# Optimization experiments

Hardware: AMD Instinct MI355X
Metric: run time of the kernel (lower is better)

Reference implementation:

```python
import jax, jax.numpy as jnp
import numpy as np

UNITS = 256
LB = -17.0
UB = 8.0
STEP = 0.05
NUM_BUCKETS = int((UB - LB) / STEP) + 1  # 501
RESIDUE = LB - STEP
W_INIT = 0.5
BATCH = 65536


def setup_inputs() -> dict:
    key = jax.random.key(0)
    kx, = jax.random.split(key, 1)
    x = jax.random.normal(kx, (BATCH, UNITS), dtype=jnp.float32)
    v = jnp.ones((UNITS, NUM_BUCKETS), dtype=jnp.float32) * W_INIT
    b = jnp.zeros((UNITS,), dtype=jnp.float32)
    return {"x": x, "v": v, "b": b}


def reference(x, v, b):
    # x: (batch, units); v: (units, num_buckets); b: (units,)
    x_clipped = jnp.clip(x, LB + 1e-9, UB - 1e-9)
    indx = ((x_clipped - LB + STEP) / STEP).astype(jnp.int32)
    indx = jnp.clip(indx, 0, NUM_BUCKETS - 1)  # (batch, units)
    delta = x_clipped - LB + STEP - indx.astype(x.dtype) * STEP

    w = jax.nn.relu(v)  # (units, num_buckets)
    # exclusive cumsum over buckets: csum[u, j] = sum_{k<j} w[u, k]
    csum = jnp.cumsum(w, axis=1)
    csum = jnp.concatenate([jnp.zeros((w.shape[0], 1), w.dtype), csum[:, :-1]], axis=1)

    unit_idx = jnp.arange(UNITS)[None, :]  # (1, units) broadcasts with indx
    csum_g = csum[unit_idx, indx]  # (batch, units)
    w_g = w[unit_idx, indx]        # (batch, units)

    # Equivalent to sum over buckets of (triangular step mask + scattered delta) * relu(v)
    logits = STEP * csum_g + delta * w_g + RESIDUE + b[None, :]
    return jax.nn.sigmoid(logits)
```

## Files before the change

kernel.cpp:

```cpp
#include <hip/hip_runtime.h>

#define UNITS 256
#define NB 501
#define STEPF 0.05f
#define LBF -17.0f
#define UBF 8.0f
#define RESIDUEF -17.05f
#define LOG2E 1.4426950408889634f

#define WLO 208
#define WSZ 224
#define UPB 32
#define PADF2 225
#define THREADS 1024
#define ROWS_PB 1024
#define CHUNKS 8

typedef float floatx4 __attribute__((ext_vector_type(4)));

__global__ __launch_bounds__(256) void build_table_kernel(
    const float* __restrict__ v, const float* __restrict__ b,
    float2* __restrict__ gtab) {
  const int lane = threadIdx.x & 63;
  const int wave = threadIdx.x >> 6;
  const int u = blockIdx.x * 4 + wave;
  if (u >= UNITS) return;

  const float* vu = v + u * NB;
  float w[8], pref[8];
  float run = 0.0f;
#pragma unroll
  for (int k = 0; k < 8; ++k) {
    const int j = lane * 8 + k;
    const float wv = (j < NB) ? fmaxf(vu[j], 0.0f) : 0.0f;
    w[k] = wv;
    pref[k] = run;
    run += wv;
  }
  float s = run;
#pragma unroll
  for (int d = 1; d < 64; d <<= 1) {
    const float o = __shfl_up(s, d, 64);
    if (lane >= d) s += o;
  }
  const float base = s - run;
  const float off = RESIDUEF + b[u];
#pragma unroll
  for (int k = 0; k < 8; ++k) {
    const int j = lane * 8 + k;
    if (j < NB) {
      const float C = STEPF * (base + pref[k]) + off - (float)j * STEPF * w[k];
      gtab[u * NB + j] = make_float2(C * LOG2E, w[k] * LOG2E);
    }
  }
}

__global__ __launch_bounds__(THREADS, 8) void iso_main_kernel(
    const float* __restrict__ x, const float2* __restrict__ gtab,
    float* __restrict__ out) {
  __shared__ float2 tab[UPB * PADF2];

  const int bu = blockIdx.x & 7;
  const int bb = blockIdx.x >> 3;
  const int u0 = bu * UPB;
  const int tid = threadIdx.x;

  {
    const int ul = tid >> 5;
    const int jt = tid & 31;
    const float2* __restrict__ src = gtab + (u0 + ul) * NB + WLO;
#pragma unroll
    for (int r = 0; r < 7; ++r) {
      const int j = jt + r * 32;
      tab[ul * PADF2 + j] = src[j];
    }
  }

  const int rowoff = tid >> 3;
  const int col4 = tid & 7;
  const floatx4* __restrict__ x4 = reinterpret_cast<const floatx4*>(x);
  floatx4* __restrict__ o4 = reinterpret_cast<floatx4*>(out);
  const int g0 = (bb * ROWS_PB + rowoff) * (UNITS / 4) + bu * (UPB / 4) + col4;
  const int gstep = 128 * (UNITS / 4);
  const int qbase = (col4 * 4) * PADF2;

  floatx4 xv[CHUNKS];
#pragma unroll
  for (int c = 0; c < CHUNKS; ++c) xv[c] = x4[g0 + c * gstep];
#pragma unroll
  for (int c = 0; c < CHUNKS; ++c) asm volatile("" : "+v"(xv[c]));

  __syncthreads();

#pragma unroll
  for (int c = 0; c < CHUNKS; ++c) {
    const floatx4 cur = xv[c];
    const float xs[4] = {cur.x, cur.y, cur.z, cur.w};
    float os[4];
#pragma unroll
    for (int k = 0; k < 4; ++k) {
      const float xc = fminf(fmaxf(xs[k], LBF + 1e-9f), UBF - 1e-9f);
      const float t = xc - LBF + STEPF;
      int idx = (int)(t * 20.0f);
      const unsigned iw = (unsigned)(idx - WLO);
      float2 cw;
      if (iw < WSZ) {
        cw = tab[qbase + k * PADF2 + (int)iw];
      } else {
        idx = idx < 0 ? 0 : (idx > NB - 1 ? NB - 1 : idx);
        cw = gtab[(u0 + col4 * 4 + k) * NB + idx];
      }
      const float l2 = fmaf(t, cw.y, cw.x);
      const float e = __builtin_amdgcn_exp2f(-l2);
      os[k] = __builtin_amdgcn_rcpf(1.0f + e);
    }
    floatx4 ov;
    ov.x = os[0]; ov.y = os[1]; ov.z = os[2]; ov.w = os[3];
    __builtin_nontemporal_store(ov, &o4[g0 + c * gstep]);
  }
}

extern "C" void kernel_launch(void* const* d_in, const int* in_sizes, int n_in,
                              void* d_out, int out_size, void* d_ws,
                              size_t ws_size, hipStream_t stream) {
  const float* x = (const float*)d_in[0];
  const float* v = (const float*)d_in[1];
  const float* b = (const float*)d_in[2];
  float* out = (float*)d_out;
  float2* gtab = (float2*)d_ws;

  build_table_kernel<<<64, 256, 0, stream>>>(v, b, gtab);

  const int rows = out_size / UNITS;
  const int grid = (UNITS / UPB) * (rows / ROWS_PB);
  iso_main_kernel<<<grid, THREADS, 0, stream>>>(x, gtab, out);
}
```

Before: 132.4 us.

## Store only cumulative sums and linearly interpolate between adjacent entries

The lookup table now holds one float per bucket (the scaled prefix sum) instead of a float2 pair of intercept and slope, and logits are formed by interpolating between neighbouring entries using the fractional part of the index. This halves table size in global and shared memory and the cost of filling the shared tile. Block size and rows per block are also halved to 512. Each evaluation now does two scalar LDS reads instead of one 8-byte read, and the interpolation may round slightly differently from the original formula.

Measured after the change: 136.7 us. 1.03x slower.

```diff
diff --git a/kernel.cpp b/kernel.cpp
--- a/kernel.cpp
+++ b/kernel.cpp
@@ -2,6 +2,7 @@
 
 #define UNITS 256
 #define NB 501
+#define NBA 502
 #define STEPF 0.05f
 #define LBF -17.0f
 #define UBF 8.0f
@@ -11,29 +12,28 @@
 #define WLO 208
 #define WSZ 224
 #define UPB 32
-#define PADF2 225
-#define THREADS 1024
-#define ROWS_PB 1024
+#define PADF 225
+#define THREADS 512
+#define ROWS_PB 512
 #define CHUNKS 8
 
 typedef float floatx4 __attribute__((ext_vector_type(4)));
 
 __global__ __launch_bounds__(256) void build_table_kernel(
     const float* __restrict__ v, const float* __restrict__ b,
-    float2* __restrict__ gtab) {
+    float* __restrict__ gtab) {
   const int lane = threadIdx.x & 63;
   const int wave = threadIdx.x >> 6;
   const int u = blockIdx.x * 4 + wave;
   if (u >= UNITS) return;
 
   const float* vu = v + u * NB;
-  float w[8], pref[8];
+  float pref[8];
   float run = 0.0f;
 #pragma unroll
   for (int k = 0; k < 8; ++k) {
     const int j = lane * 8 + k;
     const float wv = (j < NB) ? fmaxf(vu[j], 0.0f) : 0.0f;
-    w[k] = wv;
     pref[k] = run;
     run += wv;
   }
@@ -48,17 +48,16 @@
 #pragma unroll
   for (int k = 0; k < 8; ++k) {
     const int j = lane * 8 + k;
-    if (j < NB) {
-      const float C = STEPF * (base + pref[k]) + off - (float)j * STEPF * w[k];
-      gtab[u * NB + j] = make_float2(C * LOG2E, w[k] * LOG2E);
+    if (j < NBA) {
+      gtab[u * NBA + j] = (STEPF * (base + pref[k]) + off) * LOG2E;
     }
   }
 }
 
 __global__ __launch_bounds__(THREADS, 8) void iso_main_kernel(
-    const float* __restrict__ x, const float2* __restrict__ gtab,
+    const float* __restrict__ x, const float* __restrict__ gtab,
     float* __restrict__ out) {
-  __shared__ float2 tab[UPB * PADF2];
+  __shared__ float tab[UPB * PADF];
 
   const int bu = blockIdx.x & 7;
   const int bb = blockIdx.x >> 3;
@@ -66,14 +65,16 @@
   const int tid = threadIdx.x;
 
   {
-    const int ul = tid >> 5;
-    const int jt = tid & 31;
-    const float2* __restrict__ src = gtab + (u0 + ul) * NB + WLO;
+    const int ul = tid >> 4;
+    const int jt = tid & 15;
+    const float* __restrict__ src = gtab + (u0 + ul) * NBA + WLO;
+    float* __restrict__ dst = tab + ul * PADF;
 #pragma unroll
-    for (int r = 0; r < 7; ++r) {
-      const int j = jt + r * 32;
-      tab[ul * PADF2 + j] = src[j];
+    for (int r = 0; r < 14; ++r) {
+      const int j = jt + r * 16;
+      dst[j] = src[j];
     }
+    if (jt == 0) dst[224] = src[224];
   }
 
   const int rowoff = tid >> 3;
@@ -81,8 +82,8 @@
   const floatx4* __restrict__ x4 = reinterpret_cast<const floatx4*>(x);
   floatx4* __restrict__ o4 = reinterpret_cast<floatx4*>(out);
   const int g0 = (bb * ROWS_PB + rowoff) * (UNITS / 4) + bu * (UPB / 4) + col4;
-  const int gstep = 128 * (UNITS / 4);
-  const int qbase = (col4 * 4) * PADF2;
+  const int gstep = 64 * (UNITS / 4);
+  const int qrow = col4 * 4;
 
   floatx4 xv[CHUNKS];
 #pragma unroll
@@ -101,16 +102,22 @@
     for (int k = 0; k < 4; ++k) {
       const float xc = fminf(fmaxf(xs[k], LBF + 1e-9f), UBF - 1e-9f);
       const float t = xc - LBF + STEPF;
-      int idx = (int)(t * 20.0f);
+      const float ft = t * 20.0f;
+      const int idx = (int)ft;
+      const float f = ft - (float)idx;
       const unsigned iw = (unsigned)(idx - WLO);
-      float2 cw;
+      float a0, a1;
       if (iw < WSZ) {
-        cw = tab[qbase + k * PADF2 + (int)iw];
+        const float* p = &tab[qrow * PADF + k * PADF + (int)iw];
+        a0 = p[0];
+        a1 = p[1];
       } else {
-        idx = idx < 0 ? 0 : (idx > NB - 1 ? NB - 1 : idx);
-        cw = gtab[(u0 + col4 * 4 + k) * NB + idx];
+        const int ci = idx < 1 ? 1 : (idx > NB - 1 ? NB - 1 : idx);
+        const float* g = gtab + (u0 + qrow + k) * NBA + ci;
+        a0 = g[0];
+        a1 = g[1];
       }
-      const float l2 = fmaf(t, cw.y, cw.x);
+      const float l2 = fmaf(f, a1 - a0, a0);
       const float e = __builtin_amdgcn_exp2f(-l2);
       os[k] = __builtin_amdgcn_rcpf(1.0f + e);
     }
@@ -127,7 +134,7 @@
   const float* v = (const float*)d_in[1];
   const float* b = (const float*)d_in[2];
   float* out = (float*)d_out;
-  float2* gtab = (float2*)d_ws;
+  float* gtab = (float*)d_ws;
 
   build_table_kernel<<<64, 256, 0, stream>>>(v, b, gtab);
 
```
